# Kernel optimization log

Measured on AMD Instinct MI355X. Metric: run time of the kernel, lower is better.

## Reference

```python
import jax, jax.numpy as jnp
import numpy as np

N, E = 100000, 800000
D_IN, D_H, D_EMB = 64, 64, 64
L, S = 2, 4
NOISE_SCALE, MIN_U = 0.1, 1e-6


def _xavier(k, shape):
    lim = float(np.sqrt(6.0 / (shape[0] + shape[1])))
    return jax.random.uniform(k, shape, jnp.float32, -lim, lim)


def setup_inputs():
    key = jax.random.key(0)
    ks = jax.random.split(key, 7)
    x = jax.random.normal(ks[0], (N, D_IN), jnp.float32)
    edge_index = jax.random.randint(ks[1], (2, E), 0, N)
    parent_mask = jax.random.bernoulli(ks[2], 0.7, (E,))
    Wi = _xavier(ks[3], (D_IN, D_H))
    bi = jnp.zeros((D_H,), jnp.float32)
    msg_W = jnp.stack([_xavier(jax.random.fold_in(ks[4], l), (2 * D_H, D_H)) for l in range(L)])
    msg_b = jnp.zeros((L, D_H), jnp.float32)
    upd_W = jnp.stack([_xavier(jax.random.fold_in(ks[5], l), (2 * D_H, D_H)) for l in range(L)])
    upd_b = jnp.zeros((L, D_H), jnp.float32)
    Wf = _xavier(ks[6], (D_H, D_EMB))
    bf = jnp.zeros((D_EMB,), jnp.float32)
    return dict(x=x, edge_index=edge_index, parent_mask=parent_mask, Wi=Wi, bi=bi,
                msg_W=msg_W, msg_b=msg_b, upd_W=upd_W, upd_b=upd_b, Wf=Wf, bf=bf)


def _gnn(x, src, dst, mask_f, cnt_inv, Wi, bi, msg_W, msg_b, upd_W, upd_b, Wf, bf):
    # input_proj -> relu, then L rounds of (gather -> message linear -> masked
    # scatter-mean -> update linear -> relu), then final_proj.
    h = jax.nn.relu(x @ Wi + bi)
    for l in range(L):
        Wm, Wu = msg_W[l], upd_W[l]
        # message = Linear(concat(x_i, x_j)); x_i = h[dst] (target), x_j = h[src] (source)
        msg = h[dst] @ Wm[:D_H] + h[src] @ Wm[D_H:] + msg_b[l]  # [E, D_H]
        agg = jax.ops.segment_sum(msg * mask_f[:, None], dst, num_segments=N) * cnt_inv[:, None]
        # update = Linear(concat(x, aggr_out))
        h = jax.nn.relu(h @ Wu[:D_H] + agg @ Wu[D_H:] + upd_b[l])
    return h @ Wf + bf  # [N, D_EMB]


def reference(x, edge_index, parent_mask, Wi, bi, msg_W, msg_b, upd_W, upd_b, Wf, bf):
    src, dst = edge_index[0], edge_index[1]
    mask_f = parent_mask.astype(x.dtype)
    # scatter-mean over causal-parent edges only (0 for nodes without parents, as in PyG)
    cnt = jax.ops.segment_sum(mask_f, dst, num_segments=N)
    cnt_inv = 1.0 / jnp.maximum(cnt, 1.0)
    params = (Wi, bi, msg_W, msg_b, upd_W, upd_b, Wf, bf)
    causal_z = _gnn(x, src, dst, mask_f, cnt_inv, *params)
    # Monte Carlo uncertainty: S perturbed causal embeddings, trace of sample covariance
    noise = jax.random.normal(jax.random.key(42), (S, N, D_IN), x.dtype) * NOISE_SCALE
    zs = jax.lax.map(lambda n: _gnn(x + n, src, dst, mask_f, cnt_inv, *params), noise)  # [S, N, D_EMB]
    mean = zs.mean(axis=0)
    u = jnp.sum((zs - mean[None]) ** 2, axis=(0, 2)) / (S - 1)
    u = jnp.maximum(u, MIN_U)
    return causal_z, u
```

## Files before the change

kernel.cpp:

```cpp
#include <hip/hip_runtime.h>
#include <stdint.h>

#define NN 100000
#define EE 800000
#define GEMM_BX 1563
#define WSTR 72
#define SLAB ((size_t)NN * 64)
#define EDGE_CAP 2304

typedef unsigned short u16;
typedef __attribute__((ext_vector_type(8))) short bf16x8;
typedef __attribute__((ext_vector_type(4))) float f32x4;

__device__ __forceinline__ uint32_t f2bf(float f) {
  uint32_t u = __float_as_uint(f);
  return (u + 0x7fffu + ((u >> 16) & 1u)) >> 16;
}

__device__ __forceinline__ void tf_round(uint32_t& x0, uint32_t& x1, int r) {
  x0 += x1;
  x1 = (x1 << r) | (x1 >> (32 - r));
  x1 ^= x0;
}

__device__ __forceinline__ void threefry_0_42(uint32_t c0, uint32_t c1,
                                              uint32_t& o0, uint32_t& o1) {
  const uint32_t ks0 = 0u, ks1 = 42u, ks2 = 0x1BD11BDAu ^ 42u;
  uint32_t x0 = c0 + ks0, x1 = c1 + ks1;
  tf_round(x0, x1, 13); tf_round(x0, x1, 15); tf_round(x0, x1, 26); tf_round(x0, x1, 6);
  x0 += ks1; x1 += ks2 + 1u;
  tf_round(x0, x1, 17); tf_round(x0, x1, 29); tf_round(x0, x1, 16); tf_round(x0, x1, 24);
  x0 += ks2; x1 += ks0 + 2u;
  tf_round(x0, x1, 13); tf_round(x0, x1, 15); tf_round(x0, x1, 26); tf_round(x0, x1, 6);
  x0 += ks0; x1 += ks1 + 3u;
  tf_round(x0, x1, 17); tf_round(x0, x1, 29); tf_round(x0, x1, 16); tf_round(x0, x1, 24);
  x0 += ks1; x1 += ks2 + 4u;
  tf_round(x0, x1, 13); tf_round(x0, x1, 15); tf_round(x0, x1, 26); tf_round(x0, x1, 6);
  x0 += ks2; x1 += ks0 + 5u;
  o0 = x0; o1 = x1;
}

__device__ __forceinline__ float noise_val(int s, int n, int d) {
  uint32_t f = (uint32_t)s * 6400000u + (uint32_t)n * 64u + (uint32_t)d;
  uint32_t o0, o1;
  threefry_0_42(0u, f, o0, o1);
  uint32_t bits = o0 ^ o1;
  float v = __uint_as_float((bits >> 9) | 0x3f800000u) - 1.0f;
  const float LO = -0.99999994f;
  float u = v * 2.0f + LO;
  u = fmaxf(u, LO);
  float w = -__logf(fmaf(-u, u, 1.0f));
  float ww = w - 2.5f;
  float p = 2.81022636e-08f;
  p = fmaf(p, ww, 3.43273939e-07f);
  p = fmaf(p, ww, -3.5233877e-06f);
  p = fmaf(p, ww, -4.39150654e-06f);
  p = fmaf(p, ww, 0.00021858087f);
  p = fmaf(p, ww, -0.00125372503f);
  p = fmaf(p, ww, -0.00417768164f);
  p = fmaf(p, ww, 0.246640727f);
  p = fmaf(p, ww, 1.50140941f);
  if (__any(w >= 5.0f)) {
    float ws = sqrtf(w) - 3.0f;
    float p2 = -0.000200214257f;
    p2 = fmaf(p2, ws, 0.000100950558f);
    p2 = fmaf(p2, ws, 0.00134934322f);
    p2 = fmaf(p2, ws, -0.00367342844f);
    p2 = fmaf(p2, ws, 0.00573950773f);
    p2 = fmaf(p2, ws, -0.0076224613f);
    p2 = fmaf(p2, ws, 0.00943887047f);
    p2 = fmaf(p2, ws, 1.00167406f);
    p2 = fmaf(p2, ws, 2.83297682f);
    p = (w < 5.0f) ? p : p2;
  }
  return 0.141421356f * (p * u);
}

__device__ __forceinline__ int mask_at(const void* m, int e, int mode) {
  if (mode == 0) return ((const int*)m)[e] != 0;
  if (mode == 1) return ((const unsigned char*)m)[e] != 0;
  return ((const float*)m)[e] != 0.0f;
}

__global__ void k_detect(const unsigned* mw, int* mode_out) {
  __shared__ int nonbin, nonfloat;
  if (threadIdx.x == 0) { nonbin = 0; nonfloat = 0; }
  __syncthreads();
  int lb = 0, lf = 0;
  for (int i = threadIdx.x; i < 4096; i += 256) {
    unsigned v = mw[i];
    if (v > 1u) lb = 1;
    if (v != 0u && v != 0x3F800000u) lf = 1;
  }
  if (lb) atomicOr(&nonbin, 1);
  if (lf) atomicOr(&nonfloat, 1);
  __syncthreads();
  if (threadIdx.x == 0)
    mode_out[0] = (nonbin == 0) ? 0 : ((nonfloat == 0) ? 2 : 1);
}

__global__ void k_count(const void* mask, const int* dst, int* cnt, const int* mode_p) {
  int e = blockIdx.x * 256 + threadIdx.x;
  if (e >= EE) return;
  if (mask_at(mask, e, *mode_p)) atomicAdd(&cnt[dst[e]], 1);
}

__global__ void k_scan_a(const int* cnt, int* blockSums) {
  __shared__ int sd[256];
  int t = threadIdx.x;
  int base = blockIdx.x * 1024 + t * 4;
  int s = 0;
  #pragma unroll
  for (int j = 0; j < 4; ++j) {
    int i = base + j;
    if (i < NN) s += cnt[i];
  }
  sd[t] = s;
  __syncthreads();
  for (int off = 128; off > 0; off >>= 1) {
    if (t < off) sd[t] += sd[t + off];
    __syncthreads();
  }
  if (t == 0) blockSums[blockIdx.x] = sd[0];
}

__global__ void k_scan_b(int* blockSums, int nb, int* total_out) {
  __shared__ int sd[128];
  int t = threadIdx.x;
  int v = (t < nb) ? blockSums[t] : 0;
  sd[t] = v;
  __syncthreads();
  for (int off = 1; off < 128; off <<= 1) {
    int x = (t >= off) ? sd[t - off] : 0;
    __syncthreads();
    sd[t] += x;
    __syncthreads();
  }
  if (t < nb) blockSums[t] = sd[t] - v;
  if (t == 0) total_out[0] = sd[127];
}

__global__ void k_scan_c(const int* cnt, const int* blockOffs, int* row_ptr,
                         int* cursor, float* cinv) {
  __shared__ int sd[256];
  int t = threadIdx.x;
  int base = blockIdx.x * 1024 + t * 4;
  int v[4], s = 0;
  #pragma unroll
  for (int j = 0; j < 4; ++j) {
    int i = base + j;
    v[j] = (i < NN) ? cnt[i] : 0;
    s += v[j];
  }
  sd[t] = s;
  __syncthreads();
  for (int off = 1; off < 256; off <<= 1) {
    int x = (t >= off) ? sd[t - off] : 0;
    __syncthreads();
    sd[t] += x;
    __syncthreads();
  }
  int excl = sd[t] - s + blockOffs[blockIdx.x];
  #pragma unroll
  for (int j = 0; j < 4; ++j) {
    int i = base + j;
    if (i < NN) {
      row_ptr[i] = excl;
      cursor[i] = excl;
      cinv[i] = 1.0f / fmaxf((float)v[j], 1.0f);
    }
    excl += v[j];
  }
}

__global__ void k_fill(const void* mask, const int* src, const int* dst,
                       int* cursor, int* col, const int* mode_p) {
  int e = blockIdx.x * 256 + threadIdx.x;
  if (e >= EE) return;
  if (mask_at(mask, e, *mode_p)) {
    int p = atomicAdd(&cursor[dst[e]], 1);
    col[p] = src[e];
  }
}

__global__ void k_prep(const float* msg_W, const float* msg_b, const float* upd_W,
                       const float* Wi, const float* Wf,
                       u16* Wu1T, u16* A1T, u16* A2T, float* C1,
                       u16* WiT, u16* WfT) {
  int t = threadIdx.x;
  if (blockIdx.x == 2) {
    for (int o = t; o < 4096; o += 256) {
      int k = o >> 6, n = o & 63;
      WiT[n * 64 + k] = (u16)f2bf(Wi[k * 64 + n]);
      WfT[n * 64 + k] = (u16)f2bf(Wf[k * 64 + n]);
    }
    return;
  }
  int l = blockIdx.x;
  const float* WmT = msg_W + l * 8192;
  const float* WmB = WmT + 4096;
  const float* Wu1 = upd_W + l * 8192;
  const float* Wu2 = Wu1 + 4096;
  for (int o = t; o < 4096; o += 256) {
    int a = o >> 6, b = o & 63;
    float a1 = 0.f, a2 = 0.f;
    for (int j = 0; j < 64; ++j) {
      float w2 = Wu2[j * 64 + b];
      a1 = fmaf(WmT[a * 64 + j], w2, a1);
      a2 = fmaf(WmB[a * 64 + j], w2, a2);
    }
    A1T[l * 4096 + b * 64 + a]  = (u16)f2bf(a1);
    A2T[l * 4096 + b * 64 + a]  = (u16)f2bf(a2);
    Wu1T[l * 4096 + b * 64 + a] = (u16)f2bf(Wu1[a * 64 + b]);
  }
  if (t < 64) {
    float acc = 0.f;
    for (int j = 0; j < 64; ++j) acc = fmaf(msg_b[l * 64 + j], Wu2[j * 64 + t], acc);
    C1[l * 64 + t] = acc;
  }
}

__device__ __forceinline__ void mm4(const u16* lW, int m16, int q,
                                    bf16x8 a0, bf16x8 a1, f32x4 (&acc)[4]) {
  #pragma unroll
  for (int nt = 0; nt < 4; ++nt) {
    const u16* wp = lW + (nt * 16 + m16) * WSTR + q * 8;
    bf16x8 b0 = *(const bf16x8*)(wp);
    bf16x8 b1 = *(const bf16x8*)(wp + 32);
    acc[nt] = __builtin_amdgcn_mfma_f32_16x16x32_bf16(a0, b0, acc[nt], 0, 0, 0);
    acc[nt] = __builtin_amdgcn_mfma_f32_16x16x32_bf16(a1, b1, acc[nt], 0, 0, 0);
  }
}

__device__ __forceinline__ void stage_W(const u16* __restrict__ WT, u16* lW) {
  int t = threadIdx.x;
  int r = t >> 2, seg = (t & 3) * 16;
  const uint4* p = (const uint4*)(WT + r * 64 + seg);
  uint4 a = p[0], b = p[1];
  *(uint4*)(lW + r * WSTR + seg) = a;
  *(uint4*)(lW + r * WSTR + seg + 8) = b;
}

__device__ __forceinline__ void stage_H(const u16* __restrict__ Hin, int R0, u16* lT) {
  int t = threadIdx.x;
  int r = t >> 2, seg = (t & 3) * 16;
  int gr = R0 + r;
  uint4 a = {0, 0, 0, 0}, b = {0, 0, 0, 0};
  if (gr < NN) {
    const uint4* p = (const uint4*)(Hin + (size_t)gr * 64 + seg);
    a = p[0]; b = p[1];
  }
  *(uint4*)(lT + r * WSTR + seg) = a;
  *(uint4*)(lT + r * WSTR + seg + 8) = b;
}

__global__ __launch_bounds__(256) void k_input(const float* __restrict__ x,
                                               const u16* __restrict__ WiT,
                                               const float* __restrict__ bi,
                                               u16* __restrict__ HoutB) {
  __shared__ __align__(16) u16 lT[64 * WSTR];
  __shared__ __align__(16) u16 lW[64 * WSTR];
  __shared__ float lB[64];
  int t = threadIdx.x;
  int R0 = blockIdx.x * 64;
  int inst = blockIdx.y;
  u16* Hout = HoutB + (size_t)inst * SLAB;
  {
    int r = t >> 2, seg = (t & 3) * 16;
    int gr = R0 + r;
    float v[16];
    if (gr < NN) {
      const float4* xp = (const float4*)(x + (size_t)gr * 64 + seg);
      #pragma unroll
      for (int qq = 0; qq < 4; ++qq) {
        float4 f = xp[qq];
        v[qq * 4 + 0] = f.x; v[qq * 4 + 1] = f.y;
        v[qq * 4 + 2] = f.z; v[qq * 4 + 3] = f.w;
      }
      if (inst > 0) {
        int s = inst - 1;
        #pragma unroll
        for (int j = 0; j < 16; ++j) v[j] += noise_val(s, gr, seg + j);
      }
    } else {
      #pragma unroll
      for (int j = 0; j < 16; ++j) v[j] = 0.f;
    }
    uint32_t pk[8];
    #pragma unroll
    for (int j = 0; j < 8; ++j)
      pk[j] = f2bf(v[2 * j]) | (f2bf(v[2 * j + 1]) << 16);
    uint4 A = {pk[0], pk[1], pk[2], pk[3]};
    uint4 B = {pk[4], pk[5], pk[6], pk[7]};
    *(uint4*)(lT + r * WSTR + seg) = A;
    *(uint4*)(lT + r * WSTR + seg + 8) = B;
  }
  stage_W(WiT, lW);
  if (t < 64) lB[t] = bi[t];
  __syncthreads();
  int l = t & 63, w = t >> 6;
  int m16 = l & 15, q = l >> 4;
  const u16* aRow = lT + (w * 16 + m16) * WSTR + q * 8;
  bf16x8 fa0 = *(const bf16x8*)(aRow);
  bf16x8 fa1 = *(const bf16x8*)(aRow + 32);
  f32x4 acc[4] = {{0.f, 0.f, 0.f, 0.f}, {0.f, 0.f, 0.f, 0.f},
                  {0.f, 0.f, 0.f, 0.f}, {0.f, 0.f, 0.f, 0.f}};
  mm4(lW, m16, q, fa0, fa1, acc);
  #pragma unroll
  for (int nt = 0; nt < 4; ++nt) {
    int c = nt * 16 + m16;
    #pragma unroll
    for (int r_ = 0; r_ < 4; ++r_) {
      int row = w * 16 + q * 4 + r_;
      int gr = R0 + row;
      if (gr < NN) {
        float vv = fmaxf(acc[nt][r_] + lB[c], 0.f);
        Hout[(size_t)gr * 64 + c] = (u16)f2bf(vv);
      }
    }
  }
}

__global__ __launch_bounds__(256) void k_layer(const u16* __restrict__ HinB,
                                               u16* __restrict__ HoutB,
                                               const int* __restrict__ row_ptr,
                                               const int* __restrict__ col,
                                               const float* __restrict__ cinv,
                                               const u16* __restrict__ Wu1T,
                                               const u16* __restrict__ A1T,
                                               const u16* __restrict__ A2T,
                                               const float* __restrict__ b0,
                                               const float* __restrict__ c1) {
  __shared__ __align__(16) u16 lW[64 * WSTR];
  __shared__ float lB[128];
  __shared__ float lG[64];
  __shared__ int   lRP[65];
  int* lEdge = (int*)lW;

  int t = threadIdx.x;
  int R0 = blockIdx.x * 64;
  int inst = blockIdx.y;
  const u16* Hin0 = HinB + (size_t)inst * SLAB;
  u16* Hout0 = HoutB + (size_t)inst * SLAB;

  if (t < 65) {
    int idx = R0 + t;
    if (idx > NN) idx = NN;
    lRP[t] = row_ptr[idx];
  }
  if (t < 64) {
    lB[t] = b0[t];
    lB[64 + t] = c1[t];
  }
  __syncthreads();

  int e0 = lRP[0];
  int nE = lRP[64] - e0;
  bool inLds = (nE <= EDGE_CAP);
  if (inLds) {
    for (int i = t; i < nE; i += 256) lEdge[i] = col[e0 + i];
  }
  if (t < 64) lG[t] = (lRP[t + 1] > lRP[t]) ? 1.f : 0.f;
  __syncthreads();

  int l = t & 63, w = t >> 6;
  int m16 = l & 15, q = l >> 4;
  int arow = w * 16 + m16;
  int gra = R0 + arow;

  float g0[8], g1[8];
  #pragma unroll
  for (int j = 0; j < 8; ++j) { g0[j] = 0.f; g1[j] = 0.f; }
  if (gra < NN) {
    int e = lRP[arow], end = lRP[arow + 1];
    int last = end - 1;
    const u16* hq0 = Hin0 + q * 8;
    const u16* hq1 = hq0 + 32;
    for (; e < end; e += 4) {
      int idx4[4];
      #pragma unroll
      for (int j = 0; j < 4; ++j) {
        int ee = e + j;
        ee = (ee < last) ? ee : last;
        idx4[j] = inLds ? lEdge[ee - e0] : col[ee];
      }
      uint4 P0[4], P1[4];
      #pragma unroll
      for (int j = 0; j < 4; ++j) {
        size_t o = (size_t)((unsigned)idx4[j]) << 6;
        P0[j] = *(const uint4*)(hq0 + o);
        P1[j] = *(const uint4*)(hq1 + o);
      }
      #pragma unroll
      for (int j = 1; j < 4; ++j) {
        bool ok = (e + j) < end;
        P0[j].x = ok ? P0[j].x : 0u;
        P0[j].y = ok ? P0[j].y : 0u;
        P0[j].z = ok ? P0[j].z : 0u;
        P0[j].w = ok ? P0[j].w : 0u;
        P1[j].x = ok ? P1[j].x : 0u;
        P1[j].y = ok ? P1[j].y : 0u;
        P1[j].z = ok ? P1[j].z : 0u;
        P1[j].w = ok ? P1[j].w : 0u;
      }
      #pragma unroll
      for (int j = 0; j < 4; ++j) {
        uint4 v = P0[j];
        g0[0] += __uint_as_float(v.x << 16);
        g0[1] += __uint_as_float(v.x & 0xffff0000u);
        g0[2] += __uint_as_float(v.y << 16);
        g0[3] += __uint_as_float(v.y & 0xffff0000u);
        g0[4] += __uint_as_float(v.z << 16);
        g0[5] += __uint_as_float(v.z & 0xffff0000u);
        g0[6] += __uint_as_float(v.w << 16);
        g0[7] += __uint_as_float(v.w & 0xffff0000u);
        uint4 u = P1[j];
        g1[0] += __uint_as_float(u.x << 16);
        g1[1] += __uint_as_float(u.x & 0xffff0000u);
        g1[2] += __uint_as_float(u.y << 16);
        g1[3] += __uint_as_float(u.y & 0xffff0000u);
        g1[4] += __uint_as_float(u.z << 16);
        g1[5] += __uint_as_float(u.z & 0xffff0000u);
        g1[6] += __uint_as_float(u.w << 16);
        g1[7] += __uint_as_float(u.w & 0xffff0000u);
      }
    }
    float ci = cinv[gra];
    #pragma unroll
    for (int j = 0; j < 8; ++j) { g0[j] *= ci; g1[j] *= ci; }
  }

  union UB { uint32_t u[4]; bf16x8 v; };
  UB ub0, ub1;
  #pragma unroll
  for (int jj = 0; jj < 4; ++jj) {
    ub0.u[jj] = f2bf(g0[2 * jj]) | (f2bf(g0[2 * jj + 1]) << 16);
    ub1.u[jj] = f2bf(g1[2 * jj]) | (f2bf(g1[2 * jj + 1]) << 16);
  }
  bf16x8 fs0 = ub0.v, fs1 = ub1.v;

  bf16x8 zz = {0, 0, 0, 0, 0, 0, 0, 0};
  bf16x8 fa0 = zz, fa1 = zz;
  if (gra < NN) {
    const u16* ap = Hin0 + (size_t)gra * 64 + q * 8;
    fa0 = *(const bf16x8*)(ap);
    fa1 = *(const bf16x8*)(ap + 32);
  }

  __syncthreads();
  stage_W(Wu1T, lW);
  __syncthreads();

  float gA = lG[arow];
  f32x4 acc0[4] = {{0.f, 0.f, 0.f, 0.f}, {0.f, 0.f, 0.f, 0.f},
                   {0.f, 0.f, 0.f, 0.f}, {0.f, 0.f, 0.f, 0.f}};
  mm4(lW, m16, q, fa0, fa1, acc0);
  __syncthreads();
  stage_W(A1T, lW);
  __syncthreads();
  {
    bf16x8 ga0 = (gA != 0.f) ? fa0 : zz;
    bf16x8 ga1 = (gA != 0.f) ? fa1 : zz;
    mm4(lW, m16, q, ga0, ga1, acc0);
  }
  __syncthreads();
  stage_W(A2T, lW);
  __syncthreads();
  mm4(lW, m16, q, fs0, fs1, acc0);
  #pragma unroll
  for (int nt = 0; nt < 4; ++nt) {
    int c = nt * 16 + m16;
    #pragma unroll
    for (int r_ = 0; r_ < 4; ++r_) {
      int row = w * 16 + q * 4 + r_;
      int gr = R0 + row;
      if (gr < NN) {
        float bias = lB[c] + lG[row] * lB[64 + c];
        float v0 = fmaxf(acc0[nt][r_] + bias, 0.f);
        Hout0[(size_t)gr * 64 + c] = (u16)f2bf(v0);
      }
    }
  }
}

__global__ __launch_bounds__(256) void k_final(const u16* __restrict__ HinB,
                                               const u16* __restrict__ WfT,
                                               const float* __restrict__ bfv,
                                               float* __restrict__ outCausal,
                                               float* __restrict__ out_u) {
  __shared__ __align__(16) u16 lT[64 * WSTR];
  __shared__ __align__(16) u16 lW[64 * WSTR];
  __shared__ float lB[64];
  int t = threadIdx.x;
  int R0 = blockIdx.x * 64;
  stage_W(WfT, lW);
  if (t < 64) lB[t] = bfv[t];
  int l = t & 63, w = t >> 6;
  int m16 = l & 15, q = l >> 4;
  float s1[16], s2[16];
  #pragma unroll
  for (int j = 0; j < 16; ++j) { s1[j] = 0.f; s2[j] = 0.f; }

  for (int inst = 0; inst < 5; ++inst) {
    __syncthreads();
    stage_H(HinB + (size_t)inst * SLAB, R0, lT);
    __syncthreads();
    const u16* aRow = lT + (w * 16 + m16) * WSTR + q * 8;
    bf16x8 fa0 = *(const bf16x8*)(aRow);
    bf16x8 fa1 = *(const bf16x8*)(aRow + 32);
    f32x4 acc[4] = {{0.f, 0.f, 0.f, 0.f}, {0.f, 0.f, 0.f, 0.f},
                    {0.f, 0.f, 0.f, 0.f}, {0.f, 0.f, 0.f, 0.f}};
    mm4(lW, m16, q, fa0, fa1, acc);
    #pragma unroll
    for (int nt = 0; nt < 4; ++nt) {
      int c = nt * 16 + m16;
      #pragma unroll
      for (int r_ = 0; r_ < 4; ++r_) {
        float z = acc[nt][r_] + lB[c];
        if (inst == 0) {
          int gr = R0 + w * 16 + q * 4 + r_;
          if (gr < NN) outCausal[(size_t)gr * 64 + c] = z;
        } else {
          s1[nt * 4 + r_] += z;
          s2[nt * 4 + r_] = fmaf(z, z, s2[nt * 4 + r_]);
        }
      }
    }
  }
  #pragma unroll
  for (int r_ = 0; r_ < 4; ++r_) {
    float pr = 0.f;
    #pragma unroll
    for (int nt = 0; nt < 4; ++nt) {
      float a = s1[nt * 4 + r_];
      pr += s2[nt * 4 + r_] - 0.25f * a * a;
    }
    #pragma unroll
    for (int msk = 1; msk < 16; msk <<= 1)
      pr += __shfl_xor(pr, msk, 64);
    if (m16 == 0) {
      int gr = R0 + w * 16 + q * 4 + r_;
      if (gr < NN) out_u[gr] = fmaxf(pr * (1.0f / 3.0f), 1e-6f);
    }
  }
}

extern "C" void kernel_launch(void* const* d_in, const int* in_sizes, int n_in,
                              void* d_out, int out_size, void* d_ws, size_t ws_size,
                              hipStream_t stream) {
  const float* x      = (const float*)d_in[0];
  const int*   eidx   = (const int*)d_in[1];
  const void*  mask   = d_in[2];
  const float* Wi     = (const float*)d_in[3];
  const float* bi     = (const float*)d_in[4];
  const float* msg_W  = (const float*)d_in[5];
  const float* msg_b  = (const float*)d_in[6];
  const float* upd_W  = (const float*)d_in[7];
  const float* upd_b  = (const float*)d_in[8];
  const float* Wf     = (const float*)d_in[9];
  const float* bfv    = (const float*)d_in[10];

  const int* src = eidx;
  const int* dst = eidx + EE;

  char* ws = (char*)d_ws;
  size_t off = 0;
  auto alloc = [&](size_t bytes) -> void* {
    void* p = ws + off;
    off += (bytes + 255) & ~(size_t)255;
    return p;
  };

  int*   cnt     = (int*)alloc(NN * sizeof(int));
  float* cinv    = (float*)alloc(NN * sizeof(float));
  int*   row_ptr = (int*)alloc((NN + 1) * sizeof(int));
  int*   cursor  = (int*)alloc(NN * sizeof(int));
  int*   col     = (int*)alloc(EE * sizeof(int));
  int*   bsums   = (int*)alloc(128 * sizeof(int));
  int*   mode_p  = (int*)alloc(sizeof(int));
  u16*   Wu1T    = (u16*)alloc(2 * 4096 * sizeof(u16));
  u16*   A1T     = (u16*)alloc(2 * 4096 * sizeof(u16));
  u16*   A2T     = (u16*)alloc(2 * 4096 * sizeof(u16));
  u16*   WiT     = (u16*)alloc(4096 * sizeof(u16));
  u16*   WfT     = (u16*)alloc(4096 * sizeof(u16));
  float* C1      = (float*)alloc(2 * 64 * sizeof(float));
  u16*   HA      = (u16*)alloc(5 * SLAB * sizeof(u16));
  u16*   HB      = (u16*)alloc(5 * SLAB * sizeof(u16));

  float* out_causal = (float*)d_out;
  float* out_u      = (float*)d_out + SLAB;

  k_detect<<<1, 256, 0, stream>>>((const unsigned*)mask, mode_p);
  hipMemsetAsync(cnt, 0, NN * sizeof(int), stream);
  k_count<<<EE / 256, 256, 0, stream>>>(mask, dst, cnt, mode_p);
  const int SCAN_BLKS = (NN + 1023) / 1024;
  k_scan_a<<<SCAN_BLKS, 256, 0, stream>>>(cnt, bsums);
  k_scan_b<<<1, 128, 0, stream>>>(bsums, SCAN_BLKS, row_ptr + NN);
  k_scan_c<<<SCAN_BLKS, 256, 0, stream>>>(cnt, bsums, row_ptr, cursor, cinv);
  k_fill<<<EE / 256, 256, 0, stream>>>(mask, src, dst, cursor, col, mode_p);

  k_prep<<<3, 256, 0, stream>>>(msg_W, msg_b, upd_W, Wi, Wf,
                                Wu1T, A1T, A2T, C1, WiT, WfT);

  dim3 g5(GEMM_BX, 5);
  k_input<<<g5, 256, 0, stream>>>(x, WiT, bi, HA);
  k_layer<<<g5, 256, 0, stream>>>(HA, HB, row_ptr, col, cinv,
                                  Wu1T, A1T, A2T, upd_b, C1);
  k_layer<<<g5, 256, 0, stream>>>(HB, HA, row_ptr, col, cinv,
                                  Wu1T + 4096, A1T + 4096, A2T + 4096,
                                  upd_b + 64, C1 + 64);
  k_final<<<GEMM_BX, 256, 0, stream>>>(HA, WfT, bfv, out_causal, out_u);

  (void)in_sizes; (void)n_in; (void)out_size; (void)ws_size;
}
```

Baseline: 483.6 us.

## Interleave the five instances per node and remap layer blocks across XCDs

Hidden states for the five GNN instances (clean plus four noisy) now sit interleaved per node with a 320-element row stride, instead of in five separate slabs. Each gathered neighbour row then shares a contiguous region with its sibling instances. The layer kernel becomes a 1D grid whose block index is remapped so the five instances of a tile land on the same XCD (s&7), letting them share L2 for neighbour gathers. The cost is strided writes and loads in the input, layer and final kernels, plus hand-coded tile arithmetic (975 groups, tail at tile 1560) that must cover every tile exactly once.

```diff
diff --git a/kernel.cpp b/kernel.cpp
--- a/kernel.cpp
+++ b/kernel.cpp
@@ -5,8 +5,10 @@
 #define EE 800000
 #define GEMM_BX 1563
 #define WSTR 72
+#define ISTR 320
 #define SLAB ((size_t)NN * 64)
 #define EDGE_CAP 2304
+#define NBL (GEMM_BX * 5)
 
 typedef unsigned short u16;
 typedef __attribute__((ext_vector_type(8))) short bf16x8;
@@ -241,19 +243,6 @@
   *(uint4*)(lW + r * WSTR + seg + 8) = b;
 }
 
-__device__ __forceinline__ void stage_H(const u16* __restrict__ Hin, int R0, u16* lT) {
-  int t = threadIdx.x;
-  int r = t >> 2, seg = (t & 3) * 16;
-  int gr = R0 + r;
-  uint4 a = {0, 0, 0, 0}, b = {0, 0, 0, 0};
-  if (gr < NN) {
-    const uint4* p = (const uint4*)(Hin + (size_t)gr * 64 + seg);
-    a = p[0]; b = p[1];
-  }
-  *(uint4*)(lT + r * WSTR + seg) = a;
-  *(uint4*)(lT + r * WSTR + seg + 8) = b;
-}
-
 __global__ __launch_bounds__(256) void k_input(const float* __restrict__ x,
                                                const u16* __restrict__ WiT,
                                                const float* __restrict__ bi,
@@ -264,7 +253,7 @@
   int t = threadIdx.x;
   int R0 = blockIdx.x * 64;
   int inst = blockIdx.y;
-  u16* Hout = HoutB + (size_t)inst * SLAB;
+  u16* Hout = HoutB + inst * 64;
   {
     int r = t >> 2, seg = (t & 3) * 16;
     int gr = R0 + r;
@@ -315,7 +304,7 @@
       int gr = R0 + row;
       if (gr < NN) {
         float vv = fmaxf(acc[nt][r_] + lB[c], 0.f);
-        Hout[(size_t)gr * 64 + c] = (u16)f2bf(vv);
+        Hout[(size_t)gr * ISTR + c] = (u16)f2bf(vv);
       }
     }
   }
@@ -338,10 +327,20 @@
   int* lEdge = (int*)lW;
 
   int t = threadIdx.x;
-  int R0 = blockIdx.x * 64;
-  int inst = blockIdx.y;
-  const u16* Hin0 = HinB + (size_t)inst * SLAB;
-  u16* Hout0 = HoutB + (size_t)inst * SLAB;
+  int s = blockIdx.x;
+  int xcd = s & 7, g = s >> 3;
+  int tile, inst;
+  if (g < 975) {
+    tile = (g / 5) * 8 + xcd;
+    inst = g % 5;
+  } else {
+    int idx = (g - 975) * 8 + xcd;
+    tile = 1560 + idx / 5;
+    inst = idx % 5;
+  }
+  int R0 = tile * 64;
+  const u16* Hin0 = HinB + inst * 64;
+  u16* Hout0 = HoutB + inst * 64;
 
   if (t < 65) {
     int idx = R0 + t;
@@ -387,7 +386,7 @@
       uint4 P0[4], P1[4];
       #pragma unroll
       for (int j = 0; j < 4; ++j) {
-        size_t o = (size_t)((unsigned)idx4[j]) << 6;
+        size_t o = (size_t)((unsigned)idx4[j]) * ISTR;
         P0[j] = *(const uint4*)(hq0 + o);
         P1[j] = *(const uint4*)(hq1 + o);
       }
@@ -442,7 +441,7 @@
   bf16x8 zz = {0, 0, 0, 0, 0, 0, 0, 0};
   bf16x8 fa0 = zz, fa1 = zz;
   if (gra < NN) {
-    const u16* ap = Hin0 + (size_t)gra * 64 + q * 8;
+    const u16* ap = Hin0 + (size_t)gra * ISTR + q * 8;
     fa0 = *(const bf16x8*)(ap);
     fa1 = *(const bf16x8*)(ap + 32);
   }
@@ -477,7 +476,7 @@
       if (gr < NN) {
         float bias = lB[c] + lG[row] * lB[64 + c];
         float v0 = fmaxf(acc0[nt][r_] + bias, 0.f);
-        Hout0[(size_t)gr * 64 + c] = (u16)f2bf(v0);
+        Hout0[(size_t)gr * ISTR + c] = (u16)f2bf(v0);
       }
     }
   }
@@ -503,7 +502,17 @@
 
   for (int inst = 0; inst < 5; ++inst) {
     __syncthreads();
-    stage_H(HinB + (size_t)inst * SLAB, R0, lT);
+    {
+      int r = t >> 2, seg = (t & 3) * 16;
+      int gr = R0 + r;
+      uint4 a = {0, 0, 0, 0}, b = {0, 0, 0, 0};
+      if (gr < NN) {
+        const uint4* p = (const uint4*)(HinB + (size_t)gr * ISTR + inst * 64 + seg);
+        a = p[0]; b = p[1];
+      }
+      *(uint4*)(lT + r * WSTR + seg) = a;
+      *(uint4*)(lT + r * WSTR + seg + 8) = b;
+    }
     __syncthreads();
     const u16* aRow = lT + (w * 16 + m16) * WSTR + q * 8;
     bf16x8 fa0 = *(const bf16x8*)(aRow);
@@ -604,11 +613,11 @@
 
   dim3 g5(GEMM_BX, 5);
   k_input<<<g5, 256, 0, stream>>>(x, WiT, bi, HA);
-  k_layer<<<g5, 256, 0, stream>>>(HA, HB, row_ptr, col, cinv,
-                                  Wu1T, A1T, A2T, upd_b, C1);
-  k_layer<<<g5, 256, 0, stream>>>(HB, HA, row_ptr, col, cinv,
-                                  Wu1T + 4096, A1T + 4096, A2T + 4096,
-                                  upd_b + 64, C1 + 64);
+  k_layer<<<NBL, 256, 0, stream>>>(HA, HB, row_ptr, col, cinv,
+                                   Wu1T, A1T, A2T, upd_b, C1);
+  k_layer<<<NBL, 256, 0, stream>>>(HB, HA, row_ptr, col, cinv,
+                                   Wu1T + 4096, A1T + 4096, A2T + 4096,
+                                   upd_b + 64, C1 + 64);
   k_final<<<GEMM_BX, 256, 0, stream>>>(HA, WfT, bfv, out_causal, out_u);
 
   (void)in_sizes; (void)n_in; (void)out_size; (void)ws_size;
```

New measurement: 481.7 us. Within noise of the previous version (-0.4%).
